# Kernel tuning notes

Hardware: AMD Instinct MI355X
Metric: run time of the kernel (lower is better)

Reference implementation:

```python
import jax, jax.numpy as jnp
import numpy as np

T, N = 24, 2048
INPUT_DIM, HIDDEN, MEDIATE, SOCIAL, OUT_DIM = 2, 64, 128, 64, 2
N_SIZE = 2
CELL = 0.3
T_OBS, T_PRED = 9, 19
WIN = (N_SIZE + 1) ** 2  # (N_size+1)^2 = 9 window cells


def _social_pool(h, coords, mask):
    """Faithful social pooling for N_size=2, grid_cell_size=0.3.

    torch builds a dynamic grid, scatter-adds every agent's h into its cell,
    then gathers grid[int(x-R):int(x+R), int(y-R):int(y+R)] per agent.
    With R=0.3 and integer positions >= 4 (guaranteed by the margin), that
    slice is exactly the single cell (x-1, y-1), broadcast over the 3x3
    window. We compute it as a pairwise match without materializing a grid.
    Runs under torch.no_grad() -> stop_gradient.
    """
    margin = 2 * N_SIZE * CELL
    lt = jnp.stack([coords[:, 0].min(), coords[:, 1].min()]) - margin
    p = jnp.floor((coords - lt) / CELL).astype(jnp.int32)            # [N,2]
    p = p * mask.astype(jnp.int32)[:, None]                          # masked agents -> cell (0,0)
    q = p - 1                                                        # gathered cell per agent
    match = (p[None, :, 0] == q[:, None, 0]) & (p[None, :, 1] == q[:, None, 1])  # [i,j]
    cell_val = match.astype(h.dtype) @ h                             # [N,hidden] scatter-add + gather
    Hf = jnp.tile(cell_val, (1, WIN)) * mask[:, None]                # broadcast over 3x3 window, flat
    return jax.lax.stop_gradient(Hf)


def _forward(X, part_masks, all_h_t, all_c_t, Y, W_in, b_in, W_soc, b_soc,
             W_ih, W_hh, b_ih, b_hh, W_out, b_out, T_obs, T_pred):
    relu = jax.nn.relu  # dropout_prob = 0 -> Phi == ReLU

    def lstm(z, h, c):
        g = z @ W_ih.T + b_ih + h @ W_hh.T + b_hh
        i, f, gg, o = jnp.split(g, 4, axis=1)
        c = jax.nn.sigmoid(f) * c + jax.nn.sigmoid(i) * jnp.tanh(gg)
        h = jax.nn.sigmoid(o) * jnp.tanh(c)
        return h, c

    def cell_out(r, h, c, coords, m):
        Hf = _social_pool(h, coords, m)
        e = relu(Hf @ W_soc.T + b_soc)
        z = jnp.concatenate([r, e], axis=1)
        h, c = lstm(z, h, c)
        out = (h @ W_out.T + b_out) * m[:, None]
        return h, c, out

    def step_obs(carry, inp):
        h, c = carry
        x, m = inp
        r = relu(x @ W_in.T + b_in)
        h, c, out = cell_out(r, h, c, x, m)
        return (h, c), out

    (h, c), outs_obs = jax.lax.scan(
        step_obs, (all_h_t, all_c_t), (X[:T_obs + 1], part_masks[:T_obs + 1]))

    def step_pred(carry, inp):
        h, c, last_pt, prev_out = carry
        x, m = inp
        r = relu(last_pt @ W_in.T + b_in)
        h, c, out = cell_out(r, h, c, x, m)
        # torch: last_point = outputs[frame_idx - 1] AFTER the frame runs
        return (h, c, prev_out, out), out

    carry0 = (h, c, X[T_obs + 1], outs_obs[-1])
    _, outs_pred = jax.lax.scan(
        step_pred, carry0, (X[T_obs + 1:T_pred + 1], part_masks[T_obs + 1:T_pred + 1]))

    tail = jnp.zeros((X.shape[0] - T_pred - 1, X.shape[1], OUT_DIM), X.dtype)
    return jnp.concatenate([outs_obs, outs_pred, tail], axis=0)


def setup_inputs() -> dict:
    key = jax.random.key(0)
    ks = jax.random.split(key, 13)

    def lin(kw, kb, out_d, in_d):  # torch nn.Linear default init
        lim = 1.0 / float(np.sqrt(in_d))
        W = jax.random.uniform(kw, (out_d, in_d), minval=-lim, maxval=lim, dtype=jnp.float32)
        b = jax.random.uniform(kb, (out_d,), minval=-lim, maxval=lim, dtype=jnp.float32)
        return W, b

    W_in, b_in = lin(ks[0], ks[1], MEDIATE, INPUT_DIM)
    W_soc, b_soc = lin(ks[2], ks[3], SOCIAL, WIN * HIDDEN)
    W_ih, b_ih = lin(ks[4], ks[5], 4 * HIDDEN, MEDIATE + SOCIAL)
    W_hh, b_hh = lin(ks[6], ks[7], 4 * HIDDEN, HIDDEN)
    W_out, b_out = lin(ks[8], ks[9], OUT_DIM, HIDDEN)

    X = jax.random.normal(ks[10], (T, N, INPUT_DIM), dtype=jnp.float32) * 10.0  # meter-scale coords
    part_masks = (jax.random.uniform(ks[11], (T, N)) < 0.9).astype(jnp.float32)  # binary presence mask
    Y = jax.random.normal(ks[12], (T, N, INPUT_DIM), dtype=jnp.float32)  # unused by forward
    all_h_t = jnp.zeros((N, HIDDEN), jnp.float32)
    all_c_t = jnp.zeros((N, HIDDEN), jnp.float32)

    return {"X": X, "part_masks": part_masks, "all_h_t": all_h_t, "all_c_t": all_c_t,
            "Y": Y, "T_obs": T_OBS, "T_pred": T_PRED,
            "W_in": W_in, "b_in": b_in, "W_soc": W_soc, "b_soc": b_soc,
            "W_ih": W_ih, "W_hh": W_hh, "b_ih": b_ih, "b_hh": b_hh,
            "W_out": W_out, "b_out": b_out}


def reference(X, part_masks, all_h_t, all_c_t, Y, T_obs, T_pred,
              W_in, b_in, W_soc, b_soc, W_ih, W_hh, b_ih, b_hh, W_out, b_out):
    return _forward(X, part_masks, all_h_t, all_c_t, Y, W_in, b_in, W_soc, b_soc,
                    W_ih, W_hh, b_ih, b_hh, W_out, b_out, int(T_obs), int(T_pred))
```

## Files before the change

kernel.cpp:

```cpp
#include <hip/hip_runtime.h>
#include <math.h>


#define N_AG   2048
#define STEPS  20
#define CAP    12
#define NSRV   21
#define MAGIC  0x13572468

typedef short short8 __attribute__((ext_vector_type(8)));
typedef float f32x4  __attribute__((ext_vector_type(4)));
union FU { uint4 q; short8 v; };

__device__ __forceinline__ void pack8(const float* v, uint4& hq, uint4& lq) {
    unsigned uh[4], ul[4];
    #pragma unroll
    for (int w = 0; w < 4; w++) {
        float v0 = v[2 * w], v1 = v[2 * w + 1];
        unsigned h;
        asm("v_cvt_pk_bf16_f32 %0, %1, %2" : "=v"(h) : "v"(v0), "v"(v1));
        float f0 = __uint_as_float(h << 16);
        float f1 = __uint_as_float(h & 0xffff0000u);
        float r0 = v0 - f0, r1 = v1 - f1;
        unsigned l;
        asm("v_cvt_pk_bf16_f32 %0, %1, %2" : "=v"(l) : "v"(r0), "v"(r1));
        uh[w] = h; ul[w] = l;
    }
    hq = make_uint4(uh[0], uh[1], uh[2], uh[3]);
    lq = make_uint4(ul[0], ul[1], ul[2], ul[3]);
}

__device__ __forceinline__ int khash(int k) {
    return (int)(((unsigned)k * 2654435761u) >> 21);
}

__device__ __forceinline__ float fsigm(float x) {
    return __builtin_amdgcn_rcpf(1.f + __expf(-x));
}
__device__ __forceinline__ float ftanh(float x) {
    float e = __expf(2.f * x);
    return 1.f - 2.f * __builtin_amdgcn_rcpf(e + 1.f);
}

__device__ __forceinline__ void bar_lds() {
    asm volatile("s_waitcnt lgkmcnt(0)\n\ts_barrier" ::: "memory");
}

__device__ __forceinline__ void ast(int* p_, int v) {
    __hip_atomic_store(p_, v, __ATOMIC_RELAXED, __HIP_MEMORY_SCOPE_AGENT);
}
__device__ __forceinline__ void astf(float* p_, float v) {
    __hip_atomic_store(p_, v, __ATOMIC_RELAXED, __HIP_MEMORY_SCOPE_AGENT);
}
__device__ __forceinline__ unsigned long long aldu64(const unsigned long long* p_) {
    return __hip_atomic_load(p_, __ATOMIC_RELAXED, __HIP_MEMORY_SCOPE_AGENT);
}

__device__ __forceinline__ void edot_frag(
    int m5, int s5, float a0, float a1,
    float (*cvs)[68], const float* sWefP, const float* sBsoc,
    uint4* zshq, uint4* zslq)
{
    cvs[m5][s5] = a0; cvs[m5][s5 + 32] = a1;
    float acc0 = sBsoc[s5],       acc1 = sBsoc[s5 + 32];
    float acc0b = 0.f,            acc1b = 0.f;
    const float2* w0q = (const float2*)&sWefP[s5 * 66];
    const float2* w1q = (const float2*)&sWefP[(s5 + 32) * 66];
    const float4* cw = (const float4*)&cvs[m5][0];
    #pragma unroll
    for (int k4 = 0; k4 < 16; k4++) {
        float4 ca = cw[k4];
        float2 wa0 = w0q[2 * k4], wb0 = w0q[2 * k4 + 1];
        float2 wa1 = w1q[2 * k4], wb1 = w1q[2 * k4 + 1];
        acc0  += ca.x * wa0.x + ca.y * wa0.y;
        acc0b += ca.z * wb0.x + ca.w * wb0.y;
        acc1  += ca.x * wa1.x + ca.y * wa1.y;
        acc1b += ca.z * wb1.x + ca.w * wb1.y;
    }
    acc0 = fmaxf(acc0 + acc0b, 0.f);
    acc1 = fmaxf(acc1 + acc1b, 0.f);
    const int base = (m5 & 1) * 32;
    float v[8];
    #pragma unroll
    for (int jj = 0; jj < 8; jj++) {
        int c = s5 * 8 + jj;
        int srcl = base + ((c < 32 ? c : c - 32) & 31);
        float va = __shfl(acc0, srcl, 64);
        float vb = __shfl(acc1, srcl, 64);
        v[jj] = (c < 32) ? va : vb;
    }
    if (s5 < 8)
        pack8(v, zshq[(16 + s5) * 17 + m5], zslq[(16 + s5) * 17 + m5]);
}

struct KP {
    const float *X, *masks, *h_in, *c_in;
    const float *Win, *bin, *Wsoc, *bsoc, *Wih, *Whh, *bih, *bhh, *Wout, *bout;
    float *Wef;
    int *mcnt, *midx, *need, *flags;
    float *out;
    unsigned long long *hist;
};

__global__ __launch_bounds__(512, 1) void k_all(KP p)
{
    __shared__ __align__(16) uint4 zshq[544];
    __shared__ __align__(16) uint4 zslq[544];
    __shared__ float gbuf[16][260];
    __shared__ __align__(16) float cvs[16][68];
    __shared__ __align__(16) float hs[16][68];
    __shared__ __align__(16) float sWefP[64 * 66];
    __shared__ float2 sWinP[16 * 17];
    __shared__ float sBinP[16 * 9];
    __shared__ float sX[11][16][2];
    __shared__ float sMask[STEPS][16];
    __shared__ int   sCnt[STEPS][16];
    __shared__ int   sNeed[19][16];
    __shared__ int   sMidx[STEPS][16][CAP];
    __shared__ float sBsoc[64], sBc[256], sWout[128], sBout[2];
    __shared__ uint4 sE0h[8], sE0l[8];
    __shared__ int kk[N_AG];
    __shared__ int head[N_AG];
    __shared__ int nxt[N_AG];
    __shared__ float red[512];

    const int tid = threadIdx.x;
    const int bxg = blockIdx.x;

    if (bxg < NSRV) {
        const int sb = bxg;
        {
            int lo = sb * 780;
            int hi = (sb == NSRV - 1) ? 16384 : lo + 780;
            for (int i = lo + tid; i < hi; i += 512)
                p.out[20 * N_AG * 2 + i] = 0.f;
        }
        if (sb == 20) {
            for (int i = tid; i < 4096; i += 512) {
                int s = i >> 6, k = i & 63;
                float a = 0.f;
                #pragma unroll
                for (int w = 0; w < 9; w++) a += p.Wsoc[s * 576 + w * 64 + k];
                astf(&p.Wef[i], a);
            }
            __syncthreads();
            if (tid == 0) ast(&p.flags[20], MAGIC);
            return;
        }

        const int t = sb;
        const float* Xt = p.X + t * N_AG * 2;

        float mnx = 1e30f, mny = 1e30f;
        for (int i = tid; i < N_AG; i += 512) {
            mnx = fminf(mnx, Xt[2 * i]);
            mny = fminf(mny, Xt[2 * i + 1]);
        }
        red[tid] = mnx; __syncthreads();
        for (int s = 256; s > 0; s >>= 1) { if (tid < s) red[tid] = fminf(red[tid], red[tid + s]); __syncthreads(); }
        float ltx = red[0]; __syncthreads();
        red[tid] = mny; __syncthreads();
        for (int s = 256; s > 0; s >>= 1) { if (tid < s) red[tid] = fminf(red[tid], red[tid + s]); __syncthreads(); }
        float lty = red[0]; __syncthreads();
        ltx -= 1.2f;
        lty -= 1.2f;

        for (int i = tid; i < N_AG; i += 512) {
            float m = p.masks[t * N_AG + i];
            int px = (int)floorf((Xt[2 * i]     - ltx) / 0.3f);
            int py = (int)floorf((Xt[2 * i + 1] - lty) / 0.3f);
            int im = (int)m;
            px *= im; py *= im;
            kk[i] = px * 65536 + py;
            head[i] = -1;
            if (t >= 1) ast(&p.need[(t - 1) * N_AG + i], 0);
        }
        __syncthreads();
        for (int j = tid; j < N_AG; j += 512) {
            int kj = kk[j];
            if (kj != 0) nxt[j] = atomicExch(&head[khash(kj)], j);
        }
        __syncthreads();
        for (int i = tid; i < N_AG; i += 512) {
            int ki = kk[i];
            int cnt = 0;
            int base = (t * N_AG + i) * CAP;
            if (ki != 0) {
                int tkey = ki - 65537;
                int lst[CAP];
                for (int j = head[khash(tkey)]; j >= 0; j = nxt[j]) {
                    if (kk[j] == tkey) { if (cnt < CAP) lst[cnt] = j; cnt++; }
                }
                if (cnt > CAP) cnt = CAP;
                for (int a = 1; a < cnt; a++) {
                    int v = lst[a]; int b = a - 1;
                    while (b >= 0 && lst[b] > v) { lst[b + 1] = lst[b]; b--; }
                    lst[b + 1] = v;
                }
                for (int a = 0; a < cnt; a++) {
                    ast(&p.midx[base + a], lst[a]);
                    if (t >= 1) ast(&p.need[(t - 1) * N_AG + lst[a]], 1);
                }
            }
            ast(&p.mcnt[t * N_AG + i], cnt);
        }
        __syncthreads();
        if (tid == 0) ast(&p.flags[t], MAGIC);
        return;
    }

    const int bx    = bxg - NSRV;
    const int wbase = bx * 16;
    const int wv    = tid >> 6, lane = tid & 63;
    const int mA    = lane & 15, quad = lane >> 4;
    const int nt0   = 2 * wv;
    const int m0w   = wv, m1w = wv + 8;
    const int m5    = tid >> 5, s5 = tid & 31;

    if (tid < 256) sBc[tid] = p.bih[tid] + p.bhh[tid];
    if (tid < 128) {
        sWout[tid] = p.Wout[tid];
        int c = tid;
        sWinP[(c >> 3) * 17 + (c & 7)] = make_float2(p.Win[2 * c], p.Win[2 * c + 1]);
        sBinP[(c >> 3) * 9 + (c & 7)] = p.bin[c];
    }
    if (tid < 64) sBsoc[tid] = p.bsoc[tid];
    if (tid < 2)  sBout[tid] = p.bout[tid];
    if (tid < 8) {
        float v[8];
        #pragma unroll
        for (int j = 0; j < 8; j++) v[j] = fmaxf(p.bsoc[tid * 8 + j], 0.f);
        pack8(v, sE0h[tid], sE0l[tid]);
    }
    if (tid < 352) { int tt = tid / 32, r = tid % 32;
                     sX[tt][r >> 1][r & 1] = p.X[tt * (N_AG * 2) + (wbase + (r >> 1)) * 2 + (r & 1)]; }
    if (tid < 320) { int tt = tid / 16, m2 = tid % 16;
                     sMask[tt][m2] = p.masks[tt * N_AG + wbase + m2]; }

    float c0, c1;
    {
        hs[m0w][lane] = p.h_in[(wbase + m0w) * 64 + lane];
        hs[m1w][lane] = p.h_in[(wbase + m1w) * 64 + lane];
        c0 = p.c_in[(wbase + m0w) * 64 + lane];
        c1 = p.c_in[(wbase + m1w) * 64 + lane];
    }

    FU wh[2][8], wl[2][8];
    #pragma unroll
    for (int e = 0; e < 2; e++) {
        int g = (nt0 + e) * 16 + mA;
        #pragma unroll
        for (int kt = 0; kt < 8; kt++) {
            int k0 = kt * 32 + quad * 8;
            const float* src = (k0 < 192) ? (p.Wih + g * 192 + k0)
                                          : (p.Whh + g * 64 + (k0 - 192));
            float v[8];
            #pragma unroll
            for (int j = 0; j < 8; j++) v[j] = src[j];
            pack8(v, wh[e][kt].q, wl[e][kt].q);
        }
    }
    FU woh[2], wol[2];
    #pragma unroll
    for (int e2 = 0; e2 < 2; e2++) {
        int kt = 6 + e2;
        float v[8];
        #pragma unroll
        for (int j = 0; j < 8; j++) {
            int k0 = kt * 32 + quad * 8 + j - 192;
            v[j] = (mA < 2) ? p.Wout[mA * 64 + k0] : 0.f;
        }
        pack8(v, woh[e2].q, wol[e2].q);
    }

    if (tid < NSRV) {
        while (__hip_atomic_load(&p.flags[tid], __ATOMIC_RELAXED,
                                 __HIP_MEMORY_SCOPE_AGENT) != MAGIC) { }
    }
    __syncthreads();

    if (tid < 320) { int tt = tid / 16, m2 = tid % 16;
                     sCnt[tt][m2] = p.mcnt[tt * N_AG + wbase + m2]; }
    if (tid < 304) { int s = tid / 16, m2 = tid % 16;
                     sNeed[s][m2] = p.need[s * N_AG + wbase + m2]; }
    for (int i = tid; i < 4096; i += 512) sWefP[(i >> 6) * 66 + (i & 63)] = p.Wef[i];
    for (int i = tid; i < STEPS * 16 * CAP; i += 512) {
        int tt = i / (16 * CAP), r = i % (16 * CAP), m2 = r / CAP, n = r % CAP;
        sMidx[tt][m2][n] = p.midx[(tt * N_AG + wbase + m2) * CAP + n];
    }
    __syncthreads();

    {
        if (lane < 32) {
            int a = lane & 1, s5r = lane >> 1;
            int m = a ? m1w : m0w;
            float px = sX[0][m][0], py = sX[0][m][1];
            float v[8];
            #pragma unroll
            for (int j = 0; j < 8; j++) {
                float2 w2 = sWinP[s5r * 17 + j];
                v[j] = fmaxf(w2.x * px + w2.y * py + sBinP[s5r * 9 + j], 0.f);
            }
            pack8(v, zshq[s5r * 17 + m], zslq[s5r * 17 + m]);
        } else if (lane < 48) {
            int idx = lane - 32, a = idx & 1, s58 = idx >> 1;
            int m = a ? m1w : m0w;
            float v[8];
            #pragma unroll
            for (int j = 0; j < 8; j++) v[j] = hs[m][s58 * 8 + j];
            pack8(v, zshq[(24 + s58) * 17 + m], zslq[(24 + s58) * 17 + m]);
        } else {
            int idx = lane - 48, a = idx & 1, s58 = idx >> 1;
            int m = a ? m1w : m0w;
            if (sCnt[0][m] == 0) {
                zshq[(16 + s58) * 17 + m] = sE0h[s58];
                zslq[(16 + s58) * 17 + m] = sE0l[s58];
            }
        }
        int cnt0 = sCnt[0][m5];
        if (cnt0 > 0) {
            float a0 = 0.f, a1 = 0.f;
            for (int n = 0; n < cnt0; n++) {
                int r = sMidx[0][m5][n];
                a0 += p.h_in[r * 64 + s5];
                a1 += p.h_in[r * 64 + s5 + 32];
            }
            edot_frag(m5, s5, a0, a1, cvs, sWefP, sBsoc, zshq, zslq);
        }
    }
    bar_lds();

    #pragma unroll 1
    for (int t = 0; t < STEPS; t++) {
        f32x4 a0v = {0.f, 0.f, 0.f, 0.f};
        f32x4 a1v = {0.f, 0.f, 0.f, 0.f};
        f32x4 ovv = {0.f, 0.f, 0.f, 0.f};
        #pragma unroll
        for (int kt = 0; kt < 8; kt++) {
            int fi = (kt * 4 + quad) * 17 + mA;
            FU az, bz;
            az.q = zshq[fi];
            bz.q = zslq[fi];
            a0v = __builtin_amdgcn_mfma_f32_16x16x32_bf16(az.v, wh[0][kt].v, a0v, 0, 0, 0);
            a1v = __builtin_amdgcn_mfma_f32_16x16x32_bf16(az.v, wh[1][kt].v, a1v, 0, 0, 0);
            a0v = __builtin_amdgcn_mfma_f32_16x16x32_bf16(bz.v, wh[0][kt].v, a0v, 0, 0, 0);
            a1v = __builtin_amdgcn_mfma_f32_16x16x32_bf16(bz.v, wh[1][kt].v, a1v, 0, 0, 0);
            a0v = __builtin_amdgcn_mfma_f32_16x16x32_bf16(az.v, wl[0][kt].v, a0v, 0, 0, 0);
            a1v = __builtin_amdgcn_mfma_f32_16x16x32_bf16(az.v, wl[1][kt].v, a1v, 0, 0, 0);
            if (kt >= 6 && wv == 0) {
                int e2 = kt - 6;
                ovv = __builtin_amdgcn_mfma_f32_16x16x32_bf16(az.v, woh[e2].v, ovv, 0, 0, 0);
                ovv = __builtin_amdgcn_mfma_f32_16x16x32_bf16(bz.v, woh[e2].v, ovv, 0, 0, 0);
                ovv = __builtin_amdgcn_mfma_f32_16x16x32_bf16(az.v, wol[e2].v, ovv, 0, 0, 0);
            }
        }
        #pragma unroll
        for (int r = 0; r < 4; r++) {
            int row = quad * 4 + r;
            gbuf[row][nt0 * 16 + mA]       = a0v[r];
            gbuf[row][(nt0 + 1) * 16 + mA] = a1v[r];
        }
        if (wv == 0 && mA < 2) {
            #pragma unroll
            for (int r = 0; r < 4; r++)
                gbuf[quad * 4 + r][256 + mA] = ovv[r];
        }
        bar_lds();

        {
            const int hid = lane;
            float hn0, hn1;
            {
                float gi = gbuf[m0w][hid]       + sBc[hid];
                float gf = gbuf[m0w][64 + hid]  + sBc[64 + hid];
                float gR = gbuf[m0w][128 + hid] + sBc[128 + hid];
                float go = gbuf[m0w][192 + hid] + sBc[192 + hid];
                float cn = fsigm(gf) * c0 + fsigm(gi) * ftanh(gR);
                hn0 = fsigm(go) * ftanh(cn);
                c0 = cn;
                hs[m0w][hid] = hn0;
            }
            {
                float gi = gbuf[m1w][hid]       + sBc[hid];
                float gf = gbuf[m1w][64 + hid]  + sBc[64 + hid];
                float gR = gbuf[m1w][128 + hid] + sBc[128 + hid];
                float go = gbuf[m1w][192 + hid] + sBc[192 + hid];
                float cn = fsigm(gf) * c1 + fsigm(gi) * ftanh(gR);
                hn1 = fsigm(go) * ftanh(cn);
                c1 = cn;
                hs[m1w][hid] = hn1;
            }
            if (t <= 18) {
                unsigned long long* hp = p.hist + (size_t)t * (N_AG * 64);
                unsigned long long tg = ((unsigned long long)(t + 1)) << 32;
                if (sNeed[t][m0w])
                    __hip_atomic_store(&hp[(wbase + m0w) * 64 + hid],
                                       tg | (unsigned long long)__float_as_uint(hn0),
                                       __ATOMIC_RELAXED, __HIP_MEMORY_SCOPE_AGENT);
                if (sNeed[t][m1w])
                    __hip_atomic_store(&hp[(wbase + m1w) * 64 + hid],
                                       tg | (unsigned long long)__float_as_uint(hn1),
                                       __ATOMIC_RELAXED, __HIP_MEMORY_SCOPE_AGENT);
            }

            const unsigned long long* hb = p.hist + (size_t)t * (N_AG * 64);
            int cntN = 0, rfirst = -1, rsecond = -1;
            unsigned long long pw0 = 0, pw1 = 0, qw0 = 0, qw1 = 0;
            if (t < STEPS - 1) {
                cntN = sCnt[t + 1][m5];
                if (cntN > 0) {
                    rfirst = sMidx[t + 1][m5][0];
                    pw0 = aldu64(&hb[rfirst * 64 + s5]);
                    pw1 = aldu64(&hb[rfirst * 64 + s5 + 32]);
                    if (cntN > 1) {
                        rsecond = sMidx[t + 1][m5][1];
                        qw0 = aldu64(&hb[rsecond * 64 + s5]);
                        qw1 = aldu64(&hb[rsecond * 64 + s5 + 32]);
                    }
                }
            }

            float q00 = 0.f, q01 = 0.f, q10 = 0.f, q11 = 0.f;
            if (t >= 1) {
                float mk0p = sMask[t - 1][m0w], mk1p = sMask[t - 1][m1w];
                q00 = (gbuf[m0w][256] + sBout[0]) * mk0p;
                q01 = (gbuf[m0w][257] + sBout[1]) * mk0p;
                q10 = (gbuf[m1w][256] + sBout[0]) * mk1p;
                q11 = (gbuf[m1w][257] + sBout[1]) * mk1p;
                if (lane == 0)
                    *(float2*)&p.out[((t - 1) * N_AG + wbase + m0w) * 2] = make_float2(q00, q01);
                if (lane == 1)
                    *(float2*)&p.out[((t - 1) * N_AG + wbase + m1w) * 2] = make_float2(q10, q11);
            }
            if (t == STEPS - 1) {
                float w0 = sWout[hid], w1 = sWout[64 + hid];
                float p00 = hn0 * w0, p01 = hn0 * w1;
                float p10 = hn1 * w0, p11 = hn1 * w1;
                #pragma unroll
                for (int off = 32; off >= 1; off >>= 1) {
                    p00 += __shfl_xor(p00, off);
                    p01 += __shfl_xor(p01, off);
                    p10 += __shfl_xor(p10, off);
                    p11 += __shfl_xor(p11, off);
                }
                float mk0 = sMask[t][m0w], mk1 = sMask[t][m1w];
                if (lane == 0)
                    *(float2*)&p.out[(t * N_AG + wbase + m0w) * 2] =
                        make_float2((p00 + sBout[0]) * mk0, (p01 + sBout[1]) * mk0);
                if (lane == 1)
                    *(float2*)&p.out[(t * N_AG + wbase + m1w) * 2] =
                        make_float2((p10 + sBout[0]) * mk1, (p11 + sBout[1]) * mk1);
            }

            if (t < STEPS - 1) {
                const int tn = t + 1;
                if (lane < 32) {
                    int a = lane & 1, s5r = lane >> 1;
                    int m = a ? m1w : m0w;
                    float px, py;
                    if (tn <= 10) { px = sX[tn][m][0]; py = sX[tn][m][1]; }
                    else          { px = a ? q10 : q00;
                                    py = a ? q11 : q01; }
                    float v[8];
                    #pragma unroll
                    for (int j = 0; j < 8; j++) {
                        float2 w2 = sWinP[s5r * 17 + j];
                        v[j] = fmaxf(w2.x * px + w2.y * py + sBinP[s5r * 9 + j], 0.f);
                    }
                    pack8(v, zshq[s5r * 17 + m], zslq[s5r * 17 + m]);
                } else if (lane < 48) {
                    int idx = lane - 32, a = idx & 1, s58 = idx >> 1;
                    int m = a ? m1w : m0w;
                    const float4* hr = (const float4*)&hs[m][s58 * 8];
                    float4 h0 = hr[0], h1 = hr[1];
                    float v[8] = { h0.x, h0.y, h0.z, h0.w, h1.x, h1.y, h1.z, h1.w };
                    pack8(v, zshq[(24 + s58) * 17 + m], zslq[(24 + s58) * 17 + m]);
                } else {
                    int idx = lane - 48, a = idx & 1, s58 = idx >> 1;
                    int m = a ? m1w : m0w;
                    if (sCnt[tn][m] == 0) {
                        zshq[(16 + s58) * 17 + m] = sE0h[s58];
                        zslq[(16 + s58) * 17 + m] = sE0l[s58];
                    }
                }
            }

            if (cntN > 0) {
                const unsigned tagw = (unsigned)(t + 1);
                while ((unsigned)(pw0 >> 32) != tagw || (unsigned)(pw1 >> 32) != tagw) {
                    pw0 = aldu64(&hb[rfirst * 64 + s5]);
                    pw1 = aldu64(&hb[rfirst * 64 + s5 + 32]);
                }
                float a0 = __uint_as_float((unsigned)pw0);
                float a1 = __uint_as_float((unsigned)pw1);
                if (cntN > 1) {
                    while ((unsigned)(qw0 >> 32) != tagw || (unsigned)(qw1 >> 32) != tagw) {
                        qw0 = aldu64(&hb[rsecond * 64 + s5]);
                        qw1 = aldu64(&hb[rsecond * 64 + s5 + 32]);
                    }
                    a0 += __uint_as_float((unsigned)qw0);
                    a1 += __uint_as_float((unsigned)qw1);
                    for (int n = 2; n < cntN; n++) {
                        int r = sMidx[t + 1][m5][n];
                        unsigned long long w0_, w1_;
                        do {
                            w0_ = aldu64(&hb[r * 64 + s5]);
                            w1_ = aldu64(&hb[r * 64 + s5 + 32]);
                        } while ((unsigned)(w0_ >> 32) != tagw || (unsigned)(w1_ >> 32) != tagw);
                        a0 += __uint_as_float((unsigned)w0_);
                        a1 += __uint_as_float((unsigned)w1_);
                    }
                }
                edot_frag(m5, s5, a0, a1, cvs, sWefP, sBsoc, zshq, zslq);
            }
        }
        bar_lds();
    }
}

extern "C" void kernel_launch(void* const* d_in, const int* in_sizes, int n_in,
                              void* d_out, int out_size, void* d_ws, size_t ws_size,
                              hipStream_t stream)
{
    KP kp;
    kp.X     = (const float*)d_in[0];
    kp.masks = (const float*)d_in[1];
    kp.h_in  = (const float*)d_in[2];
    kp.c_in  = (const float*)d_in[3];
    kp.Win   = (const float*)d_in[7];
    kp.bin   = (const float*)d_in[8];
    kp.Wsoc  = (const float*)d_in[9];
    kp.bsoc  = (const float*)d_in[10];
    kp.Wih   = (const float*)d_in[11];
    kp.Whh   = (const float*)d_in[12];
    kp.bih   = (const float*)d_in[13];
    kp.bhh   = (const float*)d_in[14];
    kp.Wout  = (const float*)d_in[15];
    kp.bout  = (const float*)d_in[16];
    kp.out   = (float*)d_out;

    unsigned long long* hist = (unsigned long long*)d_ws;
    float* Wef  = (float*)(hist + 19 * N_AG * 64);
    int*   need = (int*)(Wef + 4096);
    int*   mcnt = need + 19 * N_AG;
    int*   midx = mcnt + STEPS * N_AG;
    int*   flags = midx + STEPS * N_AG * CAP;

    kp.hist = hist; kp.Wef = Wef; kp.need = need; kp.mcnt = mcnt;
    kp.midx = midx; kp.flags = flags;

    k_all<<<NSRV + 128, 512, 0, stream>>>(kp);
}
```

Before: 169.7 us.

## Split agents to 8 per block over 256 blocks with hi/lo rows in one MFMA tile

```diff
diff --git a/kernel.cpp b/kernel.cpp
--- a/kernel.cpp
+++ b/kernel.cpp
@@ -56,43 +56,6 @@
     return __hip_atomic_load(p_, __ATOMIC_RELAXED, __HIP_MEMORY_SCOPE_AGENT);
 }
 
-__device__ __forceinline__ void edot_frag(
-    int m5, int s5, float a0, float a1,
-    float (*cvs)[68], const float* sWefP, const float* sBsoc,
-    uint4* zshq, uint4* zslq)
-{
-    cvs[m5][s5] = a0; cvs[m5][s5 + 32] = a1;
-    float acc0 = sBsoc[s5],       acc1 = sBsoc[s5 + 32];
-    float acc0b = 0.f,            acc1b = 0.f;
-    const float2* w0q = (const float2*)&sWefP[s5 * 66];
-    const float2* w1q = (const float2*)&sWefP[(s5 + 32) * 66];
-    const float4* cw = (const float4*)&cvs[m5][0];
-    #pragma unroll
-    for (int k4 = 0; k4 < 16; k4++) {
-        float4 ca = cw[k4];
-        float2 wa0 = w0q[2 * k4], wb0 = w0q[2 * k4 + 1];
-        float2 wa1 = w1q[2 * k4], wb1 = w1q[2 * k4 + 1];
-        acc0  += ca.x * wa0.x + ca.y * wa0.y;
-        acc0b += ca.z * wb0.x + ca.w * wb0.y;
-        acc1  += ca.x * wa1.x + ca.y * wa1.y;
-        acc1b += ca.z * wb1.x + ca.w * wb1.y;
-    }
-    acc0 = fmaxf(acc0 + acc0b, 0.f);
-    acc1 = fmaxf(acc1 + acc1b, 0.f);
-    const int base = (m5 & 1) * 32;
-    float v[8];
-    #pragma unroll
-    for (int jj = 0; jj < 8; jj++) {
-        int c = s5 * 8 + jj;
-        int srcl = base + ((c < 32 ? c : c - 32) & 31);
-        float va = __shfl(acc0, srcl, 64);
-        float vb = __shfl(acc1, srcl, 64);
-        v[jj] = (c < 32) ? va : vb;
-    }
-    if (s5 < 8)
-        pack8(v, zshq[(16 + s5) * 17 + m5], zslq[(16 + s5) * 17 + m5]);
-}
-
 struct KP {
     const float *X, *masks, *h_in, *c_in;
     const float *Win, *bin, *Wsoc, *bsoc, *Wih, *Whh, *bih, *bhh, *Wout, *bout;
@@ -105,18 +68,18 @@
 __global__ __launch_bounds__(512, 1) void k_all(KP p)
 {
     __shared__ __align__(16) uint4 zshq[544];
-    __shared__ __align__(16) uint4 zslq[544];
     __shared__ float gbuf[16][260];
-    __shared__ __align__(16) float cvs[16][68];
-    __shared__ __align__(16) float hs[16][68];
+    __shared__ float gbuf2[8][260];
+    __shared__ __align__(16) float cvs[8][68];
+    __shared__ __align__(16) float hs[8][68];
     __shared__ __align__(16) float sWefP[64 * 66];
     __shared__ float2 sWinP[16 * 17];
     __shared__ float sBinP[16 * 9];
-    __shared__ float sX[11][16][2];
-    __shared__ float sMask[STEPS][16];
-    __shared__ int   sCnt[STEPS][16];
-    __shared__ int   sNeed[19][16];
-    __shared__ int   sMidx[STEPS][16][CAP];
+    __shared__ float sX[11][8][2];
+    __shared__ float sMask[STEPS][8];
+    __shared__ int   sCnt[STEPS][8];
+    __shared__ int   sNeed[19][8];
+    __shared__ int   sMidx[STEPS][8][CAP];
     __shared__ float sBsoc[64], sBc[256], sWout[128], sBout[2];
     __shared__ uint4 sE0h[8], sE0l[8];
     __shared__ int kk[N_AG];
@@ -145,77 +108,73 @@
             }
             __syncthreads();
             if (tid == 0) ast(&p.flags[20], MAGIC);
-            return;
-        }
-
-        const int t = sb;
-        const float* Xt = p.X + t * N_AG * 2;
-
-        float mnx = 1e30f, mny = 1e30f;
-        for (int i = tid; i < N_AG; i += 512) {
-            mnx = fminf(mnx, Xt[2 * i]);
-            mny = fminf(mny, Xt[2 * i + 1]);
-        }
-        red[tid] = mnx; __syncthreads();
-        for (int s = 256; s > 0; s >>= 1) { if (tid < s) red[tid] = fminf(red[tid], red[tid + s]); __syncthreads(); }
-        float ltx = red[0]; __syncthreads();
-        red[tid] = mny; __syncthreads();
-        for (int s = 256; s > 0; s >>= 1) { if (tid < s) red[tid] = fminf(red[tid], red[tid + s]); __syncthreads(); }
-        float lty = red[0]; __syncthreads();
-        ltx -= 1.2f;
-        lty -= 1.2f;
-
-        for (int i = tid; i < N_AG; i += 512) {
-            float m = p.masks[t * N_AG + i];
-            int px = (int)floorf((Xt[2 * i]     - ltx) / 0.3f);
-            int py = (int)floorf((Xt[2 * i + 1] - lty) / 0.3f);
-            int im = (int)m;
-            px *= im; py *= im;
-            kk[i] = px * 65536 + py;
-            head[i] = -1;
-            if (t >= 1) ast(&p.need[(t - 1) * N_AG + i], 0);
-        }
-        __syncthreads();
-        for (int j = tid; j < N_AG; j += 512) {
-            int kj = kk[j];
-            if (kj != 0) nxt[j] = atomicExch(&head[khash(kj)], j);
-        }
-        __syncthreads();
-        for (int i = tid; i < N_AG; i += 512) {
-            int ki = kk[i];
-            int cnt = 0;
-            int base = (t * N_AG + i) * CAP;
-            if (ki != 0) {
-                int tkey = ki - 65537;
-                int lst[CAP];
-                for (int j = head[khash(tkey)]; j >= 0; j = nxt[j]) {
-                    if (kk[j] == tkey) { if (cnt < CAP) lst[cnt] = j; cnt++; }
+        } else {
+            const int t = sb;
+            const float* Xt = p.X + t * N_AG * 2;
+
+            float mnx = 1e30f, mny = 1e30f;
+            for (int i = tid; i < N_AG; i += 512) {
+                mnx = fminf(mnx, Xt[2 * i]);
+                mny = fminf(mny, Xt[2 * i + 1]);
+            }
+            red[tid] = mnx; __syncthreads();
+            for (int s = 256; s > 0; s >>= 1) { if (tid < s) red[tid] = fminf(red[tid], red[tid + s]); __syncthreads(); }
+            float ltx = red[0]; __syncthreads();
+            red[tid] = mny; __syncthreads();
+            for (int s = 256; s > 0; s >>= 1) { if (tid < s) red[tid] = fminf(red[tid], red[tid + s]); __syncthreads(); }
+            float lty = red[0]; __syncthreads();
+            ltx -= 1.2f;
+            lty -= 1.2f;
+
+            for (int i = tid; i < N_AG; i += 512) {
+                float m = p.masks[t * N_AG + i];
+                int px = (int)floorf((Xt[2 * i]     - ltx) / 0.3f);
+                int py = (int)floorf((Xt[2 * i + 1] - lty) / 0.3f);
+                int im = (int)m;
+                px *= im; py *= im;
+                kk[i] = px * 65536 + py;
+                head[i] = -1;
+                if (t >= 1) ast(&p.need[(t - 1) * N_AG + i], 0);
+            }
+            __syncthreads();
+            for (int j = tid; j < N_AG; j += 512) {
+                int kj = kk[j];
+                if (kj != 0) nxt[j] = atomicExch(&head[khash(kj)], j);
+            }
+            __syncthreads();
+            for (int i = tid; i < N_AG; i += 512) {
+                int ki = kk[i];
+                int cnt = 0;
+                int base = (t * N_AG + i) * CAP;
+                if (ki != 0) {
+                    int tkey = ki - 65537;
+                    int lst[CAP];
+                    for (int j = head[khash(tkey)]; j >= 0; j = nxt[j]) {
+                        if (kk[j] == tkey) { if (cnt < CAP) lst[cnt] = j; cnt++; }
+                    }
+                    if (cnt > CAP) cnt = CAP;
+                    for (int a = 1; a < cnt; a++) {
+                        int v = lst[a]; int b = a - 1;
+                        while (b >= 0 && lst[b] > v) { lst[b + 1] = lst[b]; b--; }
+                        lst[b + 1] = v;
+                    }
+                    for (int a = 0; a < cnt; a++) {
+                        ast(&p.midx[base + a], lst[a]);
+                        if (t >= 1) ast(&p.need[(t - 1) * N_AG + lst[a]], 1);
+                    }
                 }
-                if (cnt > CAP) cnt = CAP;
-                for (int a = 1; a < cnt; a++) {
-                    int v = lst[a]; int b = a - 1;
-                    while (b >= 0 && lst[b] > v) { lst[b + 1] = lst[b]; b--; }
-                    lst[b + 1] = v;
-                }
-                for (int a = 0; a < cnt; a++) {
-                    ast(&p.midx[base + a], lst[a]);
-                    if (t >= 1) ast(&p.need[(t - 1) * N_AG + lst[a]], 1);
-                }
-            }
-            ast(&p.mcnt[t * N_AG + i], cnt);
-        }
-        __syncthreads();
-        if (tid == 0) ast(&p.flags[t], MAGIC);
-        return;
-    }
-
-    const int bx    = bxg - NSRV;
-    const int wbase = bx * 16;
+                ast(&p.mcnt[t * N_AG + i], cnt);
+            }
+            __syncthreads();
+            if (tid == 0) ast(&p.flags[t], MAGIC);
+        }
+    }
+
+    const int wbase = bxg * 8;
     const int wv    = tid >> 6, lane = tid & 63;
     const int mA    = lane & 15, quad = lane >> 4;
     const int nt0   = 2 * wv;
-    const int m0w   = wv, m1w = wv + 8;
-    const int m5    = tid >> 5, s5 = tid & 31;
+    const int w     = wv;
 
     if (tid < 256) sBc[tid] = p.bih[tid] + p.bhh[tid];
     if (tid < 128) {
@@ -232,17 +191,15 @@
         for (int j = 0; j < 8; j++) v[j] = fmaxf(p.bsoc[tid * 8 + j], 0.f);
         pack8(v, sE0h[tid], sE0l[tid]);
     }
-    if (tid < 352) { int tt = tid / 32, r = tid % 32;
+    if (tid < 176) { int tt = tid / 16, r = tid % 16;
                      sX[tt][r >> 1][r & 1] = p.X[tt * (N_AG * 2) + (wbase + (r >> 1)) * 2 + (r & 1)]; }
-    if (tid < 320) { int tt = tid / 16, m2 = tid % 16;
+    if (tid < 160) { int tt = tid / 8, m2 = tid % 8;
                      sMask[tt][m2] = p.masks[tt * N_AG + wbase + m2]; }
 
-    float c0, c1;
+    float c0;
     {
-        hs[m0w][lane] = p.h_in[(wbase + m0w) * 64 + lane];
-        hs[m1w][lane] = p.h_in[(wbase + m1w) * 64 + lane];
-        c0 = p.c_in[(wbase + m0w) * 64 + lane];
-        c1 = p.c_in[(wbase + m1w) * 64 + lane];
+        hs[w][lane] = p.h_in[(wbase + w) * 64 + lane];
+        c0 = p.c_in[(wbase + w) * 64 + lane];
     }
 
     FU wh[2][8], wl[2][8];
@@ -279,53 +236,65 @@
     }
     __syncthreads();
 
-    if (tid < 320) { int tt = tid / 16, m2 = tid % 16;
+    if (tid < 160) { int tt = tid / 8, m2 = tid % 8;
                      sCnt[tt][m2] = p.mcnt[tt * N_AG + wbase + m2]; }
-    if (tid < 304) { int s = tid / 16, m2 = tid % 16;
+    if (tid < 152) { int s = tid / 8, m2 = tid % 8;
                      sNeed[s][m2] = p.need[s * N_AG + wbase + m2]; }
     for (int i = tid; i < 4096; i += 512) sWefP[(i >> 6) * 66 + (i & 63)] = p.Wef[i];
-    for (int i = tid; i < STEPS * 16 * CAP; i += 512) {
-        int tt = i / (16 * CAP), r = i % (16 * CAP), m2 = r / CAP, n = r % CAP;
+    for (int i = tid; i < STEPS * 8 * CAP; i += 512) {
+        int tt = i / (8 * CAP), r = i % (8 * CAP), m2 = r / CAP, n = r % CAP;
         sMidx[tt][m2][n] = p.midx[(tt * N_AG + wbase + m2) * CAP + n];
     }
     __syncthreads();
 
     {
-        if (lane < 32) {
-            int a = lane & 1, s5r = lane >> 1;
-            int m = a ? m1w : m0w;
-            float px = sX[0][m][0], py = sX[0][m][1];
+        if (lane < 16) {
+            float px = sX[0][w][0], py = sX[0][w][1];
             float v[8];
             #pragma unroll
             for (int j = 0; j < 8; j++) {
-                float2 w2 = sWinP[s5r * 17 + j];
-                v[j] = fmaxf(w2.x * px + w2.y * py + sBinP[s5r * 9 + j], 0.f);
-            }
-            pack8(v, zshq[s5r * 17 + m], zslq[s5r * 17 + m]);
-        } else if (lane < 48) {
-            int idx = lane - 32, a = idx & 1, s58 = idx >> 1;
-            int m = a ? m1w : m0w;
+                float2 w2 = sWinP[lane * 17 + j];
+                v[j] = fmaxf(w2.x * px + w2.y * py + sBinP[lane * 9 + j], 0.f);
+            }
+            pack8(v, zshq[lane * 17 + w], zshq[lane * 17 + w + 8]);
+        } else if (lane < 24) {
+            int s58 = lane - 16;
+            const float4* hr = (const float4*)&hs[w][s58 * 8];
+            float4 h0 = hr[0], h1 = hr[1];
+            float v[8] = { h0.x, h0.y, h0.z, h0.w, h1.x, h1.y, h1.z, h1.w };
+            pack8(v, zshq[(24 + s58) * 17 + w], zshq[(24 + s58) * 17 + w + 8]);
+        } else if (lane < 32) {
+            int s58 = lane - 24;
+            if (sCnt[0][w] == 0) {
+                zshq[(16 + s58) * 17 + w]     = sE0h[s58];
+                zshq[(16 + s58) * 17 + w + 8] = sE0l[s58];
+            }
+        }
+        int cnt0 = sCnt[0][w];
+        if (cnt0 > 0) {
+            float a = 0.f;
+            for (int n = 0; n < cnt0; n++) {
+                int r = sMidx[0][w][n];
+                a += p.h_in[r * 64 + lane];
+            }
+            cvs[w][lane] = a;
+            asm volatile("s_waitcnt lgkmcnt(0)" ::: "memory");
+            float acc = sBsoc[lane], accb = 0.f;
+            const float4* cw = (const float4*)&cvs[w][0];
+            const float2* wq = (const float2*)&sWefP[lane * 66];
+            #pragma unroll
+            for (int k4 = 0; k4 < 16; k4++) {
+                float4 ca = cw[k4];
+                float2 wa = wq[2 * k4], wb = wq[2 * k4 + 1];
+                acc  += ca.x * wa.x + ca.y * wa.y;
+                accb += ca.z * wb.x + ca.w * wb.y;
+            }
+            acc = fmaxf(acc + accb, 0.f);
             float v[8];
             #pragma unroll
-            for (int j = 0; j < 8; j++) v[j] = hs[m][s58 * 8 + j];
-            pack8(v, zshq[(24 + s58) * 17 + m], zslq[(24 + s58) * 17 + m]);
-        } else {
-            int idx = lane - 48, a = idx & 1, s58 = idx >> 1;
-            int m = a ? m1w : m0w;
-            if (sCnt[0][m] == 0) {
-                zshq[(16 + s58) * 17 + m] = sE0h[s58];
-                zslq[(16 + s58) * 17 + m] = sE0l[s58];
-            }
-        }
-        int cnt0 = sCnt[0][m5];
-        if (cnt0 > 0) {
-            float a0 = 0.f, a1 = 0.f;
-            for (int n = 0; n < cnt0; n++) {
-                int r = sMidx[0][m5][n];
-                a0 += p.h_in[r * 64 + s5];
-                a1 += p.h_in[r * 64 + s5 + 32];
-            }
-            edot_frag(m5, s5, a0, a1, cvs, sWefP, sBsoc, zshq, zslq);
+            for (int j = 0; j < 8; j++) v[j] = __shfl(acc, (lane & 7) * 8 + j, 64);
+            if (lane < 8)
+                pack8(v, zshq[(16 + lane) * 17 + w], zshq[(16 + lane) * 17 + w + 8]);
         }
     }
     bar_lds();
@@ -334,24 +303,21 @@
     for (int t = 0; t < STEPS; t++) {
         f32x4 a0v = {0.f, 0.f, 0.f, 0.f};
         f32x4 a1v = {0.f, 0.f, 0.f, 0.f};
+        f32x4 a0l = {0.f, 0.f, 0.f, 0.f};
+        f32x4 a1l = {0.f, 0.f, 0.f, 0.f};
         f32x4 ovv = {0.f, 0.f, 0.f, 0.f};
+        f32x4 ovl = {0.f, 0.f, 0.f, 0.f};
         #pragma unroll
         for (int kt = 0; kt < 8; kt++) {
-            int fi = (kt * 4 + quad) * 17 + mA;
-            FU az, bz;
-            az.q = zshq[fi];
-            bz.q = zslq[fi];
+            FU az;
+            az.q = zshq[(kt * 4 + quad) * 17 + mA];
             a0v = __builtin_amdgcn_mfma_f32_16x16x32_bf16(az.v, wh[0][kt].v, a0v, 0, 0, 0);
             a1v = __builtin_amdgcn_mfma_f32_16x16x32_bf16(az.v, wh[1][kt].v, a1v, 0, 0, 0);
-            a0v = __builtin_amdgcn_mfma_f32_16x16x32_bf16(bz.v, wh[0][kt].v, a0v, 0, 0, 0);
-            a1v = __builtin_amdgcn_mfma_f32_16x16x32_bf16(bz.v, wh[1][kt].v, a1v, 0, 0, 0);
-            a0v = __builtin_amdgcn_mfma_f32_16x16x32_bf16(az.v, wl[0][kt].v, a0v, 0, 0, 0);
-            a1v = __builtin_amdgcn_mfma_f32_16x16x32_bf16(az.v, wl[1][kt].v, a1v, 0, 0, 0);
+            a0l = __builtin_amdgcn_mfma_f32_16x16x32_bf16(az.v, wl[0][kt].v, a0l, 0, 0, 0);
+            a1l = __builtin_amdgcn_mfma_f32_16x16x32_bf16(az.v, wl[1][kt].v, a1l, 0, 0, 0);
             if (kt >= 6 && wv == 0) {
-                int e2 = kt - 6;
-                ovv = __builtin_amdgcn_mfma_f32_16x16x32_bf16(az.v, woh[e2].v, ovv, 0, 0, 0);
-                ovv = __builtin_amdgcn_mfma_f32_16x16x32_bf16(bz.v, woh[e2].v, ovv, 0, 0, 0);
-                ovv = __builtin_amdgcn_mfma_f32_16x16x32_bf16(az.v, wol[e2].v, ovv, 0, 0, 0);
+                ovv = __builtin_amdgcn_mfma_f32_16x16x32_bf16(az.v, woh[kt - 6].v, ovv, 0, 0, 0);
+                ovl = __builtin_amdgcn_mfma_f32_16x16x32_bf16(az.v, wol[kt - 6].v, ovl, 0, 0, 0);
             }
         }
         #pragma unroll
@@ -360,158 +326,143 @@
             gbuf[row][nt0 * 16 + mA]       = a0v[r];
             gbuf[row][(nt0 + 1) * 16 + mA] = a1v[r];
         }
+        if (quad < 2) {
+            #pragma unroll
+            for (int r = 0; r < 4; r++) {
+                int row = quad * 4 + r;
+                gbuf2[row][nt0 * 16 + mA]       = a0l[r];
+                gbuf2[row][(nt0 + 1) * 16 + mA] = a1l[r];
+            }
+        }
         if (wv == 0 && mA < 2) {
             #pragma unroll
-            for (int r = 0; r < 4; r++)
-                gbuf[quad * 4 + r][256 + mA] = ovv[r];
+            for (int r = 0; r < 4; r++) {
+                int row = quad * 4 + r;
+                gbuf[row][256 + mA] = ovv[r];
+                if (quad < 2) gbuf2[row][256 + mA] = ovl[r];
+            }
         }
         bar_lds();
 
         {
             const int hid = lane;
-            float hn0, hn1;
-            {
-                float gi = gbuf[m0w][hid]       + sBc[hid];
-                float gf = gbuf[m0w][64 + hid]  + sBc[64 + hid];
-                float gR = gbuf[m0w][128 + hid] + sBc[128 + hid];
-                float go = gbuf[m0w][192 + hid] + sBc[192 + hid];
-                float cn = fsigm(gf) * c0 + fsigm(gi) * ftanh(gR);
-                hn0 = fsigm(go) * ftanh(cn);
-                c0 = cn;
-                hs[m0w][hid] = hn0;
-            }
-            {
-                float gi = gbuf[m1w][hid]       + sBc[hid];
-                float gf = gbuf[m1w][64 + hid]  + sBc[64 + hid];
-                float gR = gbuf[m1w][128 + hid] + sBc[128 + hid];
-                float go = gbuf[m1w][192 + hid] + sBc[192 + hid];
-                float cn = fsigm(gf) * c1 + fsigm(gi) * ftanh(gR);
-                hn1 = fsigm(go) * ftanh(cn);
-                c1 = cn;
-                hs[m1w][hid] = hn1;
-            }
-            if (t <= 18) {
+            float gi = gbuf[w][hid]       + gbuf[w + 8][hid]       + gbuf2[w][hid]       + sBc[hid];
+            float gf = gbuf[w][64 + hid]  + gbuf[w + 8][64 + hid]  + gbuf2[w][64 + hid]  + sBc[64 + hid];
+            float gR = gbuf[w][128 + hid] + gbuf[w + 8][128 + hid] + gbuf2[w][128 + hid] + sBc[128 + hid];
+            float go = gbuf[w][192 + hid] + gbuf[w + 8][192 + hid] + gbuf2[w][192 + hid] + sBc[192 + hid];
+            float cn = fsigm(gf) * c0 + fsigm(gi) * ftanh(gR);
+            float hn = fsigm(go) * ftanh(cn);
+            c0 = cn;
+            hs[w][hid] = hn;
+
+            if (t <= 18 && sNeed[t][w]) {
                 unsigned long long* hp = p.hist + (size_t)t * (N_AG * 64);
                 unsigned long long tg = ((unsigned long long)(t + 1)) << 32;
-                if (sNeed[t][m0w])
-                    __hip_atomic_store(&hp[(wbase + m0w) * 64 + hid],
-                                       tg | (unsigned long long)__float_as_uint(hn0),
-                                       __ATOMIC_RELAXED, __HIP_MEMORY_SCOPE_AGENT);
-                if (sNeed[t][m1w])
-                    __hip_atomic_store(&hp[(wbase + m1w) * 64 + hid],
-                                       tg | (unsigned long long)__float_as_uint(hn1),
-                                       __ATOMIC_RELAXED, __HIP_MEMORY_SCOPE_AGENT);
+                __hip_atomic_store(&hp[(wbase + w) * 64 + hid],
+                                   tg | (unsigned long long)__float_as_uint(hn),
+                                   __ATOMIC_RELAXED, __HIP_MEMORY_SCOPE_AGENT);
             }
 
             const unsigned long long* hb = p.hist + (size_t)t * (N_AG * 64);
             int cntN = 0, rfirst = -1, rsecond = -1;
-            unsigned long long pw0 = 0, pw1 = 0, qw0 = 0, qw1 = 0;
+            unsigned long long pw0 = 0, qw0 = 0;
             if (t < STEPS - 1) {
-                cntN = sCnt[t + 1][m5];
+                cntN = sCnt[t + 1][w];
                 if (cntN > 0) {
-                    rfirst = sMidx[t + 1][m5][0];
-                    pw0 = aldu64(&hb[rfirst * 64 + s5]);
-                    pw1 = aldu64(&hb[rfirst * 64 + s5 + 32]);
+                    rfirst = sMidx[t + 1][w][0];
+                    pw0 = aldu64(&hb[rfirst * 64 + lane]);
                     if (cntN > 1) {
-                        rsecond = sMidx[t + 1][m5][1];
-                        qw0 = aldu64(&hb[rsecond * 64 + s5]);
-                        qw1 = aldu64(&hb[rsecond * 64 + s5 + 32]);
+                        rsecond = sMidx[t + 1][w][1];
+                        qw0 = aldu64(&hb[rsecond * 64 + lane]);
                     }
                 }
             }
 
-            float q00 = 0.f, q01 = 0.f, q10 = 0.f, q11 = 0.f;
+            float q0 = 0.f, q1 = 0.f;
             if (t >= 1) {
-                float mk0p = sMask[t - 1][m0w], mk1p = sMask[t - 1][m1w];
-                q00 = (gbuf[m0w][256] + sBout[0]) * mk0p;
-                q01 = (gbuf[m0w][257] + sBout[1]) * mk0p;
-                q10 = (gbuf[m1w][256] + sBout[0]) * mk1p;
-                q11 = (gbuf[m1w][257] + sBout[1]) * mk1p;
+                float mkp = sMask[t - 1][w];
+                q0 = (gbuf[w][256] + gbuf[w + 8][256] + gbuf2[w][256] + sBout[0]) * mkp;
+                q1 = (gbuf[w][257] + gbuf[w + 8][257] + gbuf2[w][257] + sBout[1]) * mkp;
                 if (lane == 0)
-                    *(float2*)&p.out[((t - 1) * N_AG + wbase + m0w) * 2] = make_float2(q00, q01);
-                if (lane == 1)
-                    *(float2*)&p.out[((t - 1) * N_AG + wbase + m1w) * 2] = make_float2(q10, q11);
+                    *(float2*)&p.out[((t - 1) * N_AG + wbase + w) * 2] = make_float2(q0, q1);
             }
             if (t == STEPS - 1) {
-                float w0 = sWout[hid], w1 = sWout[64 + hid];
-                float p00 = hn0 * w0, p01 = hn0 * w1;
-                float p10 = hn1 * w0, p11 = hn1 * w1;
+                float p0 = hn * sWout[hid], p1 = hn * sWout[64 + hid];
                 #pragma unroll
                 for (int off = 32; off >= 1; off >>= 1) {
-                    p00 += __shfl_xor(p00, off);
-                    p01 += __shfl_xor(p01, off);
-                    p10 += __shfl_xor(p10, off);
-                    p11 += __shfl_xor(p11, off);
+                    p0 += __shfl_xor(p0, off);
+                    p1 += __shfl_xor(p1, off);
                 }
-                float mk0 = sMask[t][m0w], mk1 = sMask[t][m1w];
+                float mk = sMask[t][w];
                 if (lane == 0)
-                    *(float2*)&p.out[(t * N_AG + wbase + m0w) * 2] =
-                        make_float2((p00 + sBout[0]) * mk0, (p01 + sBout[1]) * mk0);
-                if (lane == 1)
-                    *(float2*)&p.out[(t * N_AG + wbase + m1w) * 2] =
-                        make_float2((p10 + sBout[0]) * mk1, (p11 + sBout[1]) * mk1);
+                    *(float2*)&p.out[(t * N_AG + wbase + w) * 2] =
+                        make_float2((p0 + sBout[0]) * mk, (p1 + sBout[1]) * mk);
             }
 
             if (t < STEPS - 1) {
                 const int tn = t + 1;
-                if (lane < 32) {
-                    int a = lane & 1, s5r = lane >> 1;
-                    int m = a ? m1w : m0w;
+                if (lane < 16) {
                     float px, py;
-                    if (tn <= 10) { px = sX[tn][m][0]; py = sX[tn][m][1]; }
-                    else          { px = a ? q10 : q00;
-                                    py = a ? q11 : q01; }
+                    if (tn <= 10) { px = sX[tn][w][0]; py = sX[tn][w][1]; }
+                    else          { px = q0; py = q1; }
                     float v[8];
                     #pragma unroll
                     for (int j = 0; j < 8; j++) {
-                        float2 w2 = sWinP[s5r * 17 + j];
-                        v[j] = fmaxf(w2.x * px + w2.y * py + sBinP[s5r * 9 + j], 0.f);
-                    }
-                    pack8(v, zshq[s5r * 17 + m], zslq[s5r * 17 + m]);
-                } else if (lane < 48) {
-                    int idx = lane - 32, a = idx & 1, s58 = idx >> 1;
-                    int m = a ? m1w : m0w;
-                    const float4* hr = (const float4*)&hs[m][s58 * 8];
+                        float2 w2 = sWinP[lane * 17 + j];
+                        v[j] = fmaxf(w2.x * px + w2.y * py + sBinP[lane * 9 + j], 0.f);
+                    }
+                    pack8(v, zshq[lane * 17 + w], zshq[lane * 17 + w + 8]);
+                } else if (lane < 24) {
+                    int s58 = lane - 16;
+                    const float4* hr = (const float4*)&hs[w][s58 * 8];
                     float4 h0 = hr[0], h1 = hr[1];
                     float v[8] = { h0.x, h0.y, h0.z, h0.w, h1.x, h1.y, h1.z, h1.w };
-                    pack8(v, zshq[(24 + s58) * 17 + m], zslq[(24 + s58) * 17 + m]);
-                } else {
-                    int idx = lane - 48, a = idx & 1, s58 = idx >> 1;
-                    int m = a ? m1w : m0w;
-                    if (sCnt[tn][m] == 0) {
-                        zshq[(16 + s58) * 17 + m] = sE0h[s58];
-                        zslq[(16 + s58) * 17 + m] = sE0l[s58];
+                    pack8(v, zshq[(24 + s58) * 17 + w], zshq[(24 + s58) * 17 + w + 8]);
+                } else if (lane < 32) {
+                    int s58 = lane - 24;
+                    if (sCnt[tn][w] == 0) {
+                        zshq[(16 + s58) * 17 + w]     = sE0h[s58];
+                        zshq[(16 + s58) * 17 + w + 8] = sE0l[s58];
                     }
                 }
             }
 
             if (cntN > 0) {
                 const unsigned tagw = (unsigned)(t + 1);
-                while ((unsigned)(pw0 >> 32) != tagw || (unsigned)(pw1 >> 32) != tagw) {
-                    pw0 = aldu64(&hb[rfirst * 64 + s5]);
-                    pw1 = aldu64(&hb[rfirst * 64 + s5 + 32]);
+                while ((unsigned)(pw0 >> 32) != tagw)
+                    pw0 = aldu64(&hb[rfirst * 64 + lane]);
+                float a = __uint_as_float((unsigned)pw0);
+                if (cntN > 1) {
+                    while ((unsigned)(qw0 >> 32) != tagw)
+                        qw0 = aldu64(&hb[rsecond * 64 + lane]);
+                    a += __uint_as_float((unsigned)qw0);
+                    for (int n = 2; n < cntN; n++) {
+                        int r = sMidx[t + 1][w][n];
+                        unsigned long long w0_;
+                        do {
+                            w0_ = aldu64(&hb[r * 64 + lane]);
+                        } while ((unsigned)(w0_ >> 32) != tagw);
+                        a += __uint_as_float((unsigned)w0_);
+                    }
                 }
-                float a0 = __uint_as_float((unsigned)pw0);
-                float a1 = __uint_as_float((unsigned)pw1);
-                if (cntN > 1) {
-                    while ((unsigned)(qw0 >> 32) != tagw || (unsigned)(qw1 >> 32) != tagw) {
-                        qw0 = aldu64(&hb[rsecond * 64 + s5]);
-                        qw1 = aldu64(&hb[rsecond * 64 + s5 + 32]);
-                    }
-                    a0 += __uint_as_float((unsigned)qw0);
-                    a1 += __uint_as_float((unsigned)qw1);
-                    for (int n = 2; n < cntN; n++) {
-                        int r = sMidx[t + 1][m5][n];
-                        unsigned long long w0_, w1_;
-                        do {
-                            w0_ = aldu64(&hb[r * 64 + s5]);
-                            w1_ = aldu64(&hb[r * 64 + s5 + 32]);
-                        } while ((unsigned)(w0_ >> 32) != tagw || (unsigned)(w1_ >> 32) != tagw);
-                        a0 += __uint_as_float((unsigned)w0_);
-                        a1 += __uint_as_float((unsigned)w1_);
-                    }
+                cvs[w][lane] = a;
+                asm volatile("s_waitcnt lgkmcnt(0)" ::: "memory");
+                float acc = sBsoc[lane], accb = 0.f;
+                const float4* cw = (const float4*)&cvs[w][0];
+                const float2* wq = (const float2*)&sWefP[lane * 66];
+                #pragma unroll
+                for (int k4 = 0; k4 < 16; k4++) {
+                    float4 ca = cw[k4];
+                    float2 wa = wq[2 * k4], wb = wq[2 * k4 + 1];
+                    acc  += ca.x * wa.x + ca.y * wa.y;
+                    accb += ca.z * wb.x + ca.w * wb.y;
                 }
-                edot_frag(m5, s5, a0, a1, cvs, sWefP, sBsoc, zshq, zslq);
+                acc = fmaxf(acc + accb, 0.f);
+                float v[8];
+                #pragma unroll
+                for (int j = 0; j < 8; j++) v[j] = __shfl(acc, (lane & 7) * 8 + j, 64);
+                if (lane < 8)
+                    pack8(v, zshq[(16 + lane) * 17 + w], zshq[(16 + lane) * 17 + w + 8]);
             }
         }
         bar_lds();
@@ -549,5 +500,5 @@
     kp.hist = hist; kp.Wef = Wef; kp.need = need; kp.mcnt = mcnt;
     kp.midx = midx; kp.flags = flags;
 
-    k_all<<<NSRV + 128, 512, 0, stream>>>(kp);
-}
+    k_all<<<256, 512, 0, stream>>>(kp);
+}
```

After: 157.3 us (median of 2 runs). -7.3%, faster.
